# Performance work log

Measured on AMD Instinct MI355X. Metric: run time of the kernel, lower is better.

## Reference

```python
import jax, jax.numpy as jnp
import numpy as np

ALPHA_LIM = (float(np.exp(-1.0 / 5.0)), float(np.exp(-1.0 / 25.0)))
BETA_LIM = (float(np.exp(-1.0 / 30.0)), float(np.exp(-1.0 / 120.0)))
A_LIM = (-1.0, 1.0)
B_LIM = (0.0, 2.0)
THRESHOLD = 1.0


@jax.custom_vjp
def spike_boxcar(x):
    # Heaviside forward, boxcar surrogate gradient
    return (x > 0).astype(x.dtype)


def _spike_fwd(x):
    return spike_boxcar(x), x


def _spike_bwd(x, g):
    return (jnp.where(jnp.abs(x) <= 0.5, g, jnp.zeros_like(g)),)


spike_boxcar.defvjp(_spike_fwd, _spike_bwd)


def setup_inputs() -> dict:
    key = jax.random.key(0)
    ks = jax.random.split(key, 9)
    B, T, I, H = 128, 512, 512, 512
    return {
        "x": jax.random.normal(ks[0], (B, T, I), dtype=jnp.float32),
        "W": jax.random.normal(ks[1], (H, I), dtype=jnp.float32) / np.sqrt(I),
        "alpha": jax.random.uniform(ks[2], (H,), dtype=jnp.float32),
        "beta": jax.random.uniform(ks[3], (H,), dtype=jnp.float32),
        "a": jax.random.uniform(ks[4], (H,), dtype=jnp.float32),
        "b": jax.random.uniform(ks[5], (H,), dtype=jnp.float32),
        "u0": jax.random.uniform(ks[6], (B, H), dtype=jnp.float32),
        "w0": jax.random.uniform(ks[7], (B, H), dtype=jnp.float32),
        "s0": jax.random.uniform(ks[8], (B, H), dtype=jnp.float32),
    }


def reference(x, W, alpha, beta, a, b, u0, w0, s0):
    # x: [B, T, I]; W: [H, I] (nn.Linear weight, no bias)
    alpha = jnp.clip(alpha, ALPHA_LIM[0], ALPHA_LIM[1])
    beta = jnp.clip(beta, BETA_LIM[0], BETA_LIM[1])
    a = jnp.clip(a, A_LIM[0], A_LIM[1])
    b = jnp.clip(b, B_LIM[0], B_LIM[1])

    Wx = jnp.einsum("bti,hi->bth", x, W)  # [B, T, H]
    Wx_t = jnp.transpose(Wx, (1, 0, 2))    # [T, B, H] for scan over time

    def step(carry, wx_t):
        ut, wt, st = carry
        wt = beta * wt + a * ut + b * st
        ut = alpha * (ut - st) + (1.0 - alpha) * (wx_t - wt)
        st = spike_boxcar(ut - THRESHOLD)
        return (ut, wt, st), st

    _, s = jax.lax.scan(step, (u0, w0, s0), Wx_t)  # s: [T, B, H]
    return jnp.transpose(s, (1, 0, 2))  # [B, T, H]
```

## Files before the change

kernel.cpp:

```cpp
#include <hip/hip_runtime.h>
#include <hip/hip_bf16.h>


#define M_SZ 65536
#define H_SZ 512
#define K_SZ 512
#define B_SZ 128
#define T_SZ 512
#define LSTR 132

typedef __attribute__((ext_vector_type(4))) float f32x4;

__device__ __forceinline__ bool detect_bf16(const unsigned int* __restrict__ w) {
  int c = 0;
#pragma unroll
  for (int i = 0; i < 64; ++i) {
    unsigned int e = (w[i] >> 7) & 0xffu;
    c += (e >= 115u && e <= 131u) ? 1 : 0;
  }
  return c > 32;
}

template <bool ISB>
__device__ __forceinline__ f32x4 ld4t(const void* __restrict__ p, size_t off) {
  if constexpr (!ISB) {
    return *reinterpret_cast<const f32x4*>(reinterpret_cast<const float*>(p) + off);
  } else {
    uint2 v = *reinterpret_cast<const uint2*>(reinterpret_cast<const unsigned short*>(p) + off);
    f32x4 r;
    r.x = __uint_as_float((v.x & 0xffffu) << 16);
    r.y = __uint_as_float(v.x & 0xffff0000u);
    r.z = __uint_as_float((v.y & 0xffffu) << 16);
    r.w = __uint_as_float(v.y & 0xffff0000u);
    return r;
  }
}

template <bool ISB>
__device__ __forceinline__ float ld1t(const void* __restrict__ p, int i) {
  if constexpr (!ISB) return reinterpret_cast<const float*>(p)[i];
  return __uint_as_float((unsigned int)(reinterpret_cast<const unsigned short*>(p)[i]) << 16);
}

template <bool ISB>
__device__ __forceinline__ void gemm_body(const void* __restrict__ X,
                                          const void* __restrict__ Wm,
                                          float* __restrict__ C,
                                          float* __restrict__ As,
                                          float* __restrict__ Bs) {
  const int tid = threadIdx.x;
  const int r0 = tid >> 2;
  const int q0 = (tid & 3) * 4;
  const int tx = tid & 15;
  const int ty = tid >> 4;
  const size_t M0 = (size_t)(blockIdx.x >> 2) * 128;
  const int N0 = (blockIdx.x & 3) * 128;

  float acc[8][8];
#pragma unroll
  for (int i = 0; i < 8; ++i)
#pragma unroll
    for (int j = 0; j < 8; ++j) acc[i][j] = 0.0f;

  const size_t aoff0 = (M0 + r0) * K_SZ + q0;
  const size_t aoff1 = (M0 + r0 + 64) * K_SZ + q0;
  const size_t boff0 = (size_t)(N0 + r0) * K_SZ + q0;
  const size_t boff1 = (size_t)(N0 + r0 + 64) * K_SZ + q0;

  f32x4 pa0 = ld4t<ISB>(X, aoff0), pa1 = ld4t<ISB>(X, aoff1);
  f32x4 pb0 = ld4t<ISB>(Wm, boff0), pb1 = ld4t<ISB>(Wm, boff1);

  for (int kk = 0; kk < K_SZ; kk += 16) {
    __syncthreads();
    As[(q0 + 0) * LSTR + r0] = pa0.x; As[(q0 + 1) * LSTR + r0] = pa0.y;
    As[(q0 + 2) * LSTR + r0] = pa0.z; As[(q0 + 3) * LSTR + r0] = pa0.w;
    As[(q0 + 0) * LSTR + r0 + 64] = pa1.x; As[(q0 + 1) * LSTR + r0 + 64] = pa1.y;
    As[(q0 + 2) * LSTR + r0 + 64] = pa1.z; As[(q0 + 3) * LSTR + r0 + 64] = pa1.w;
    Bs[(q0 + 0) * LSTR + r0] = pb0.x; Bs[(q0 + 1) * LSTR + r0] = pb0.y;
    Bs[(q0 + 2) * LSTR + r0] = pb0.z; Bs[(q0 + 3) * LSTR + r0] = pb0.w;
    Bs[(q0 + 0) * LSTR + r0 + 64] = pb1.x; Bs[(q0 + 1) * LSTR + r0 + 64] = pb1.y;
    Bs[(q0 + 2) * LSTR + r0 + 64] = pb1.z; Bs[(q0 + 3) * LSTR + r0 + 64] = pb1.w;
    __syncthreads();
    if (kk + 16 < K_SZ) {
      pa0 = ld4t<ISB>(X, aoff0 + kk + 16); pa1 = ld4t<ISB>(X, aoff1 + kk + 16);
      pb0 = ld4t<ISB>(Wm, boff0 + kk + 16); pb1 = ld4t<ISB>(Wm, boff1 + kk + 16);
    }
#pragma unroll
    for (int k = 0; k < 16; ++k) {
      const f32x4 a0 = *reinterpret_cast<const f32x4*>(As + k * LSTR + ty * 4);
      const f32x4 a1 = *reinterpret_cast<const f32x4*>(As + k * LSTR + 64 + ty * 4);
      const f32x4 b0 = *reinterpret_cast<const f32x4*>(Bs + k * LSTR + tx * 4);
      const f32x4 b1 = *reinterpret_cast<const f32x4*>(Bs + k * LSTR + 64 + tx * 4);
      const float av[8] = {a0.x, a0.y, a0.z, a0.w, a1.x, a1.y, a1.z, a1.w};
      const float bv[8] = {b0.x, b0.y, b0.z, b0.w, b1.x, b1.y, b1.z, b1.w};
#pragma unroll
      for (int i = 0; i < 8; ++i)
#pragma unroll
        for (int j = 0; j < 8; ++j) acc[i][j] += av[i] * bv[j];
    }
  }

  const int b = (int)(M0 >> 9);
  const int t0b = (int)(M0 & 511);
#pragma unroll
  for (int j = 0; j < 8; ++j) {
    const int n = N0 + ((j < 4) ? (tx * 4 + j) : (64 + tx * 4 + (j - 4)));
    float* cp = C + ((size_t)b * H_SZ + n) * T_SZ + t0b;
    f32x4 vlo = {acc[0][j], acc[1][j], acc[2][j], acc[3][j]};
    f32x4 vhi = {acc[4][j], acc[5][j], acc[6][j], acc[7][j]};
    *reinterpret_cast<f32x4*>(cp + ty * 4) = vlo;
    *reinterpret_cast<f32x4*>(cp + 64 + ty * 4) = vhi;
  }
}

__global__ __launch_bounds__(256) void sgemm_bt(const void* __restrict__ X,
                                                const void* __restrict__ Wm,
                                                float* __restrict__ C) {
  __shared__ float As[16 * LSTR];
  __shared__ float Bs[16 * LSTR];
  if (detect_bf16(reinterpret_cast<const unsigned int*>(X)))
    gemm_body<true>(X, Wm, C, As, Bs);
  else
    gemm_body<false>(X, Wm, C, As, Bs);
}

template <bool ISB>
__device__ __forceinline__ void scan_body(
    const float* __restrict__ wxT, const void* __restrict__ alpha_p,
    const void* __restrict__ beta_p, const void* __restrict__ a_p,
    const void* __restrict__ b_p, const void* __restrict__ u0p,
    const void* __restrict__ w0p, const void* __restrict__ s0p,
    void* __restrict__ out) {
  const int tid = threadIdx.x;
  const int bb = blockIdx.x >> 2;
  const int quarter = blockIdx.x & 3;
  const int h = quarter * 128 + tid;

  const float al = fminf(fmaxf(ld1t<ISB>(alpha_p, h), (float)0.8187307530779818),
                         (float)0.9607894391523232);
  const float be = fminf(fmaxf(ld1t<ISB>(beta_p, h), (float)0.9672161004820059),
                         (float)0.9917013044213351);
  const float av = fminf(fmaxf(ld1t<ISB>(a_p, h), -1.0f), 1.0f);
  const float bv = fminf(fmaxf(ld1t<ISB>(b_p, h), 0.0f), 2.0f);
  const float om = __fsub_rn(1.0f, al);

  const int bh = bb * H_SZ + h;
  float u = ld1t<ISB>(u0p, bh);
  float w = ld1t<ISB>(w0p, bh);
  float s = ld1t<ISB>(s0p, bh);

  const float* base = wxT + ((size_t)bb * H_SZ + h) * T_SZ;
  float* outf = reinterpret_cast<float*>(out);
  __hip_bfloat16* outb = reinterpret_cast<__hip_bfloat16*>(out);
  const size_t ob0 = (size_t)bb * T_SZ * H_SZ + h;

  f32x4 ring[8];
#pragma unroll
  for (int c = 0; c < 4; ++c) {
    ring[2 * c] = *reinterpret_cast<const f32x4*>(base + c * 8);
    ring[2 * c + 1] = *reinterpret_cast<const f32x4*>(base + c * 8 + 4);
  }

  for (int c0 = 0; c0 < T_SZ / 8; c0 += 4) {
#pragma unroll
    for (int c2 = 0; c2 < 4; ++c2) {
      const int c = c0 + c2;
      const f32x4 v0 = ring[2 * c2];
      const f32x4 v1 = ring[2 * c2 + 1];
      if (c + 4 < T_SZ / 8) {
        ring[2 * c2] = *reinterpret_cast<const f32x4*>(base + (c + 4) * 8);
        ring[2 * c2 + 1] = *reinterpret_cast<const f32x4*>(base + (c + 4) * 8 + 4);
      }
      const float cur[8] = {v0.x, v0.y, v0.z, v0.w, v1.x, v1.y, v1.z, v1.w};
#pragma unroll
      for (int j = 0; j < 8; ++j) {
        w = __fadd_rn(__fadd_rn(__fmul_rn(be, w), __fmul_rn(av, u)), __fmul_rn(bv, s));
        u = __fadd_rn(__fmul_rn(al, __fsub_rn(u, s)), __fmul_rn(om, __fsub_rn(cur[j], w)));
        s = (u > 1.0f) ? 1.0f : 0.0f;
        const size_t o = ob0 + (size_t)(c * 8 + j) * H_SZ;
        if constexpr (ISB) outb[o] = __float2bfloat16(s);
        else outf[o] = s;
      }
    }
  }
}

__global__ __launch_bounds__(128) void lif_scan(
    const float* __restrict__ wxT, const void* __restrict__ X,
    const void* __restrict__ alpha_p, const void* __restrict__ beta_p,
    const void* __restrict__ a_p, const void* __restrict__ b_p,
    const void* __restrict__ u0p, const void* __restrict__ w0p,
    const void* __restrict__ s0p, void* __restrict__ out) {
  if (detect_bf16(reinterpret_cast<const unsigned int*>(X)))
    scan_body<true>(wxT, alpha_p, beta_p, a_p, b_p, u0p, w0p, s0p, out);
  else
    scan_body<false>(wxT, alpha_p, beta_p, a_p, b_p, u0p, w0p, s0p, out);
}

extern "C" void kernel_launch(void* const* d_in, const int* in_sizes, int n_in,
                              void* d_out, int out_size, void* d_ws, size_t ws_size,
                              hipStream_t stream) {
  const void* X = d_in[0];
  const void* Wm = d_in[1];
  float* ws = reinterpret_cast<float*>(d_ws);

  sgemm_bt<<<dim3((M_SZ / 128) * (H_SZ / 128)), dim3(256), 0, stream>>>(X, Wm, ws);

  lif_scan<<<dim3(B_SZ * 4), dim3(128), 0, stream>>>(
      ws, X, d_in[2], d_in[3], d_in[4], d_in[5], d_in[6], d_in[7], d_in[8], d_out);
}
```

Baseline: 729.5 us.

## Store GEMM output row-major and stream scan inputs via async global-to-LDS ring

The GEMM epilogue now writes Wx in natural [B,T,H] order with nontemporal vector stores instead of the transposed [B,H,T] layout. The scan kernel then reads those rows as coalesced chunks, loaded asynchronously into a 4-slot shared-memory ring with global_load_lds, three chunks ahead, and synchronised with hand-written s_waitcnt and barrier. This targets the strided, poorly coalesced transposed writes in the GEMM and the per-thread strided loads in the scan. In exchange it adds 64KB of LDS per scan block and relies on a vmcnt threshold, which is fragile because the per-step output stores also count against vmcnt.

```diff
diff --git a/kernel.cpp b/kernel.cpp
--- a/kernel.cpp
+++ b/kernel.cpp
@@ -40,6 +40,12 @@
 __device__ __forceinline__ float ld1t(const void* __restrict__ p, int i) {
   if constexpr (!ISB) return reinterpret_cast<const float*>(p)[i];
   return __uint_as_float((unsigned int)(reinterpret_cast<const unsigned short*>(p)[i]) << 16);
+}
+
+__device__ __forceinline__ void gl_lds16(const void* g, void* l) {
+  __builtin_amdgcn_global_load_lds(
+      (const __attribute__((address_space(1))) void*)g,
+      (__attribute__((address_space(3))) void*)l, 16, 0, 0);
 }
 
 template <bool ISB>
@@ -100,16 +106,14 @@
     }
   }
 
-  const int b = (int)(M0 >> 9);
-  const int t0b = (int)(M0 & 511);
-#pragma unroll
-  for (int j = 0; j < 8; ++j) {
-    const int n = N0 + ((j < 4) ? (tx * 4 + j) : (64 + tx * 4 + (j - 4)));
-    float* cp = C + ((size_t)b * H_SZ + n) * T_SZ + t0b;
-    f32x4 vlo = {acc[0][j], acc[1][j], acc[2][j], acc[3][j]};
-    f32x4 vhi = {acc[4][j], acc[5][j], acc[6][j], acc[7][j]};
-    *reinterpret_cast<f32x4*>(cp + ty * 4) = vlo;
-    *reinterpret_cast<f32x4*>(cp + 64 + ty * 4) = vhi;
+#pragma unroll
+  for (int r = 0; r < 8; ++r) {
+    const size_t m = M0 + ((r < 4) ? (ty * 4 + r) : (64 + ty * 4 + (r - 4)));
+    float* Cp = C + m * H_SZ + N0;
+    f32x4 v0 = {acc[r][0], acc[r][1], acc[r][2], acc[r][3]};
+    f32x4 v1 = {acc[r][4], acc[r][5], acc[r][6], acc[r][7]};
+    __builtin_nontemporal_store(v0, reinterpret_cast<f32x4*>(Cp + tx * 4));
+    __builtin_nontemporal_store(v1, reinterpret_cast<f32x4*>(Cp + 64 + tx * 4));
   }
 }
 
@@ -124,14 +128,21 @@
     gemm_body<false>(X, Wm, C, As, Bs);
 }
 
+#define SCH 32
+#define NCH (T_SZ / SCH)
+#define NSLOT 4
+#define LOOKA 3
+
 template <bool ISB>
 __device__ __forceinline__ void scan_body(
-    const float* __restrict__ wxT, const void* __restrict__ alpha_p,
+    const float* __restrict__ wx, const void* __restrict__ alpha_p,
     const void* __restrict__ beta_p, const void* __restrict__ a_p,
     const void* __restrict__ b_p, const void* __restrict__ u0p,
     const void* __restrict__ w0p, const void* __restrict__ s0p,
-    void* __restrict__ out) {
+    void* __restrict__ out, float* __restrict__ ring) {
   const int tid = threadIdx.x;
+  const int wv = tid >> 6;
+  const int lane = tid & 63;
   const int bb = blockIdx.x >> 2;
   const int quarter = blockIdx.x & 3;
   const int h = quarter * 128 + tid;
@@ -149,52 +160,51 @@
   float w = ld1t<ISB>(w0p, bh);
   float s = ld1t<ISB>(s0p, bh);
 
-  const float* base = wxT + ((size_t)bb * H_SZ + h) * T_SZ;
+  const float* xb = wx + (size_t)bb * T_SZ * H_SZ + quarter * 128;
   float* outf = reinterpret_cast<float*>(out);
   __hip_bfloat16* outb = reinterpret_cast<__hip_bfloat16*>(out);
   const size_t ob0 = (size_t)bb * T_SZ * H_SZ + h;
 
-  f32x4 ring[8];
-#pragma unroll
-  for (int c = 0; c < 4; ++c) {
-    ring[2 * c] = *reinterpret_cast<const f32x4*>(base + c * 8);
-    ring[2 * c + 1] = *reinterpret_cast<const f32x4*>(base + c * 8 + 4);
-  }
-
-  for (int c0 = 0; c0 < T_SZ / 8; c0 += 4) {
-#pragma unroll
-    for (int c2 = 0; c2 < 4; ++c2) {
-      const int c = c0 + c2;
-      const f32x4 v0 = ring[2 * c2];
-      const f32x4 v1 = ring[2 * c2 + 1];
-      if (c + 4 < T_SZ / 8) {
-        ring[2 * c2] = *reinterpret_cast<const f32x4*>(base + (c + 4) * 8);
-        ring[2 * c2 + 1] = *reinterpret_cast<const f32x4*>(base + (c + 4) * 8 + 4);
-      }
-      const float cur[8] = {v0.x, v0.y, v0.z, v0.w, v1.x, v1.y, v1.z, v1.w};
-#pragma unroll
-      for (int j = 0; j < 8; ++j) {
-        w = __fadd_rn(__fadd_rn(__fmul_rn(be, w), __fmul_rn(av, u)), __fmul_rn(bv, s));
-        u = __fadd_rn(__fmul_rn(al, __fsub_rn(u, s)), __fmul_rn(om, __fsub_rn(cur[j], w)));
-        s = (u > 1.0f) ? 1.0f : 0.0f;
-        const size_t o = ob0 + (size_t)(c * 8 + j) * H_SZ;
-        if constexpr (ISB) outb[o] = __float2bfloat16(s);
-        else outf[o] = s;
-      }
+  auto issue = [&](int c) {
+    float* dst = ring + (c & (NSLOT - 1)) * (SCH * 128) + wv * (16 * 128);
+    const float* sp = xb + (size_t)(c * SCH + wv * 16) * H_SZ;
+#pragma unroll
+    for (int i = 0; i < 8; ++i) {
+      gl_lds16(sp + (size_t)(2 * i + (lane >> 5)) * H_SZ + (lane & 31) * 4,
+               dst + 2 * i * 128);
+    }
+  };
+
+  issue(0); issue(1); issue(2);
+
+  for (int c = 0; c < NCH; ++c) {
+    if (c + LOOKA < NCH) issue(c + LOOKA);
+    asm volatile("s_waitcnt vmcnt(24)\n\ts_barrier" ::: "memory");
+    const float* cb = ring + (c & (NSLOT - 1)) * (SCH * 128);
+#pragma unroll 8
+    for (int j = 0; j < SCH; ++j) {
+      const float cur = cb[j * 128 + tid];
+      w = __fadd_rn(__fadd_rn(__fmul_rn(be, w), __fmul_rn(av, u)), __fmul_rn(bv, s));
+      u = __fadd_rn(__fmul_rn(al, __fsub_rn(u, s)), __fmul_rn(om, __fsub_rn(cur, w)));
+      s = (u > 1.0f) ? 1.0f : 0.0f;
+      const size_t o = ob0 + (size_t)(c * SCH + j) * H_SZ;
+      if constexpr (ISB) outb[o] = __float2bfloat16(s);
+      else outf[o] = s;
     }
   }
 }
 
 __global__ __launch_bounds__(128) void lif_scan(
-    const float* __restrict__ wxT, const void* __restrict__ X,
+    const float* __restrict__ wx, const void* __restrict__ X,
     const void* __restrict__ alpha_p, const void* __restrict__ beta_p,
     const void* __restrict__ a_p, const void* __restrict__ b_p,
     const void* __restrict__ u0p, const void* __restrict__ w0p,
     const void* __restrict__ s0p, void* __restrict__ out) {
+  __shared__ float ring[NSLOT * SCH * 128];
   if (detect_bf16(reinterpret_cast<const unsigned int*>(X)))
-    scan_body<true>(wxT, alpha_p, beta_p, a_p, b_p, u0p, w0p, s0p, out);
+    scan_body<true>(wx, alpha_p, beta_p, a_p, b_p, u0p, w0p, s0p, out, ring);
   else
-    scan_body<false>(wxT, alpha_p, beta_p, a_p, b_p, u0p, w0p, s0p, out);
+    scan_body<false>(wx, alpha_p, beta_p, a_p, b_p, u0p, w0p, s0p, out, ring);
 }
 
 extern "C" void kernel_launch(void* const* d_in, const int* in_sizes, int n_in,
```

Result: faster. 648.6 us (-11.1%).
